# Kernel optimization log

Measured on AMD Instinct MI355X. Metric: run time of the kernel, lower is better.

## Reference

```python
import jax, jax.numpy as jnp
import numpy as np

B, S, H = 2, 2048, 4096
NQ, NKV, D = 32, 8, 128
EPS = 1e-6
THETA = 1000000.0


def rms_norm(x, w, eps=EPS):
    # normalize over last dim (per-head RMSNorm on head_dim)
    var = jnp.mean(jnp.square(x), axis=-1, keepdims=True)
    return x * jax.lax.rsqrt(var + eps) * w


def rope(x, positions, theta=THETA):
    # x: [B, S, N, D]; rotate-half convention (Qwen/Llama style)
    d = x.shape[-1]
    inv_freq = 1.0 / (theta ** (jnp.arange(0, d, 2, dtype=jnp.float32) / d))  # [D/2]
    ang = positions[:, None].astype(jnp.float32) * inv_freq[None, :]          # [S, D/2]
    cos = jnp.cos(ang)[None, :, None, :]
    sin = jnp.sin(ang)[None, :, None, :]
    x1, x2 = x[..., : d // 2], x[..., d // 2 :]
    return jnp.concatenate([x1 * cos - x2 * sin, x2 * cos + x1 * sin], axis=-1)


def setup_inputs() -> dict:
    key = jax.random.key(0)
    ks = jax.random.split(key, 7)
    sc_in = 1.0 / np.sqrt(H)
    sc_out = 1.0 / np.sqrt(NQ * D)
    return {
        "x": jax.random.normal(ks[0], (B, S, H), jnp.float32),
        "wq": jax.random.normal(ks[1], (H, NQ * D), jnp.float32) * sc_in,
        "wk": jax.random.normal(ks[2], (H, NKV * D), jnp.float32) * sc_in,
        "wv": jax.random.normal(ks[3], (H, NKV * D), jnp.float32) * sc_in,
        "wo": jax.random.normal(ks[4], (NQ * D, H), jnp.float32) * sc_out,
        "q_norm_w": jnp.ones((D,), jnp.float32),
        "k_norm_w": jnp.ones((D,), jnp.float32),
    }


def reference(x, wq, wk, wv, wo, q_norm_w, k_norm_w):
    b, s, _ = x.shape
    positions = jnp.arange(s)

    q = (x @ wq).reshape(b, s, NQ, D)   # [B,S,NQ,D]
    k = (x @ wk).reshape(b, s, NKV, D)  # [B,S,NKV,D]
    v = (x @ wv).reshape(b, s, NKV, D)

    # per-head QK RMSNorm, then RoPE
    q = rope(rms_norm(q, q_norm_w), positions)
    k = rope(rms_norm(k, k_norm_w), positions)

    # GQA: expand kv heads to query heads (group = NQ // NKV)
    g = NQ // NKV
    k = jnp.repeat(k, g, axis=2)  # [B,S,NQ,D]
    v = jnp.repeat(v, g, axis=2)

    scale = D ** -0.5
    scores = jnp.einsum("bqhd,bkhd->bhqk", q, k) * scale  # [B,NQ,S,S]
    causal = jnp.tril(jnp.ones((s, s), bool))
    scores = jnp.where(causal[None, None], scores, jnp.finfo(scores.dtype).min)
    attn = jax.nn.softmax(scores, axis=-1)

    out = jnp.einsum("bhqk,bkhd->bqhd", attn, v).reshape(b, s, NQ * D)
    return out @ wo
```

## Files before the change

### kernel.cpp

```cpp
#include <hip/hip_runtime.h>
#include <hip/hip_bf16.h>

#define DEV __device__ __forceinline__

typedef unsigned short u16;
typedef unsigned int u32;
typedef __attribute__((ext_vector_type(8))) short short8;
typedef __attribute__((ext_vector_type(4))) float f32x4;
typedef __attribute__((ext_vector_type(16))) float f32x16;

static constexpr int Bb = 2, Ss = 2048, Hh = 4096, NQ = 32, NKV = 8, Dd = 128;
static constexpr int Mm = Bb * Ss;

DEV u16 f2bf(float f) {
    u32 u = __float_as_uint(f);
    u32 r = (u + 0x7fffu + ((u >> 16) & 1u)) >> 16;
    return (u16)r;
}
DEV float bf2f(u16 b) { return __uint_as_float((u32)b << 16); }
DEV u32 cvtpk(float lo, float hi) {
    u32 r;
    asm("v_cvt_pk_bf16_f32 %0, %1, %2" : "=v"(r) : "v"(lo), "v"(hi));
    return r;
}

__global__ void k_cast(const float4* __restrict__ in, ushort4* __restrict__ out, int n4) {
    int i = blockIdx.x * 256 + threadIdx.x;
    if (i < n4) {
        float4 v = in[i];
        ushort4 o;
        o.x = f2bf(v.x); o.y = f2bf(v.y); o.z = f2bf(v.z); o.w = f2bf(v.w);
        out[i] = o;
    }
}

__global__ void k_transpose(const float* __restrict__ in, u16* __restrict__ out, int R, int C) {
    __shared__ float t[32][33];
    int lx = threadIdx.x & 31, ly = threadIdx.x >> 5;
    long tc = (long)blockIdx.x * 32, tr = (long)blockIdx.y * 32;
    #pragma unroll
    for (int i = 0; i < 32; i += 8) t[ly + i][lx] = in[(tr + ly + i) * C + tc + lx];
    __syncthreads();
    #pragma unroll
    for (int i = 0; i < 32; i += 8) out[(tc + ly + i) * R + tr + lx] = f2bf(t[lx][ly + i]);
}

DEV void gld16(const void* g, void* l) {
    __builtin_amdgcn_global_load_lds((const __attribute__((address_space(1))) void*)g,
                                     (__attribute__((address_space(3))) void*)l, 16, 0, 0);
}

#define FENCE asm volatile("" ::: "memory")

template <int MODE>
__global__ __launch_bounds__(512) void k_gemm256(const u16* __restrict__ A, const u16* __restrict__ BT,
                                                 void* __restrict__ Cp, int M, int N, int K) {
    __shared__ u16 S[2][32768];
    const int tid = threadIdx.x, lane = tid & 63, wid = tid >> 6;
    const int wr = wid >> 2, wc = wid & 3;
    const long m0 = (long)blockIdx.y * 256, n0 = (long)blockIdx.x * 256;
    const int r15 = lane & 15;
    const int cch0 = 8 * ((lane >> 4) ^ (r15 & 7));

    const u16 *pA[4], *pB[4];
    {
        int srow = wid * 8 + (lane >> 3);
        int scol = 8 * ((lane & 7) ^ (lane >> 3));
        #pragma unroll
        for (int j = 0; j < 4; j++) {
            pA[j] = A + (m0 + j * 64 + srow) * (long)K + scol;
            pB[j] = BT + (n0 + j * 64 + srow) * (long)K + scol;
        }
    }

    f32x4 acc[8][4];
    #pragma unroll
    for (int i = 0; i < 8; i++)
        #pragma unroll
        for (int j = 0; j < 4; j++) acc[i][j] = f32x4{0.f, 0.f, 0.f, 0.f};

    const int NT = K / 64;
    auto STAGE_A = [&](int t) {
        int tb = t & 1; long ko = (long)t * 64;
        #pragma unroll
        for (int j = 0; j < 4; j++) gld16(pA[j] + ko, (void*)&S[tb][j * 4096 + wid * 512]);
    };
    auto STAGE_B = [&](int t) {
        int tb = t & 1; long ko = (long)t * 64;
        #pragma unroll
        for (int j = 0; j < 4; j++) gld16(pB[j] + ko, (void*)&S[tb][16384 + j * 4096 + wid * 512]);
    };

    const int aro = wr * 8192 + r15 * 64 + cch0;
    const int bro = 16384 + (wc >> 1) * 8192 + (wc & 1) * 4096 + r15 * 64 + cch0;

    STAGE_B(0); STAGE_A(0); STAGE_B(1); STAGE_A(1);
    asm volatile("s_waitcnt vmcnt(8)" ::: "memory");
    FENCE; __builtin_amdgcn_s_barrier(); FENCE;

    short8 af[4][2], b01[2][2], b23[2][2];
    for (int kt = 0; kt < NT; ++kt) {
        const u16* Sb = S[kt & 1];
        #pragma unroll
        for (int m = 0; m < 4; m++) {
            af[m][0] = *(const short8*)&Sb[aro + m * 1024];
            af[m][1] = *(const short8*)&Sb[(aro + m * 1024) ^ 32];
        }
        #pragma unroll
        for (int n = 0; n < 2; n++) {
            b01[n][0] = *(const short8*)&Sb[bro + n * 1024];
            b01[n][1] = *(const short8*)&Sb[(bro + n * 1024) ^ 32];
        }
        FENCE; __builtin_amdgcn_s_barrier(); FENCE;
        __builtin_amdgcn_s_setprio(1);
        #pragma unroll
        for (int m = 0; m < 4; m++)
            #pragma unroll
            for (int n = 0; n < 2; n++) {
                acc[m][n] = __builtin_amdgcn_mfma_f32_16x16x32_bf16(af[m][0], b01[n][0], acc[m][n], 0, 0, 0);
                acc[m][n] = __builtin_amdgcn_mfma_f32_16x16x32_bf16(af[m][1], b01[n][1], acc[m][n], 0, 0, 0);
            }
        __builtin_amdgcn_s_setprio(0);
        FENCE; __builtin_amdgcn_s_barrier(); FENCE;
        #pragma unroll
        for (int n = 0; n < 2; n++) {
            b23[n][0] = *(const short8*)&Sb[bro + (n + 2) * 1024];
            b23[n][1] = *(const short8*)&Sb[(bro + (n + 2) * 1024) ^ 32];
        }
        FENCE; __builtin_amdgcn_s_barrier(); FENCE;
        __builtin_amdgcn_s_setprio(1);
        #pragma unroll
        for (int m = 0; m < 4; m++)
            #pragma unroll
            for (int n = 0; n < 2; n++) {
                acc[m][n + 2] = __builtin_amdgcn_mfma_f32_16x16x32_bf16(af[m][0], b23[n][0], acc[m][n + 2], 0, 0, 0);
                acc[m][n + 2] = __builtin_amdgcn_mfma_f32_16x16x32_bf16(af[m][1], b23[n][1], acc[m][n + 2], 0, 0, 0);
            }
        __builtin_amdgcn_s_setprio(0);
        FENCE; __builtin_amdgcn_s_barrier(); FENCE;
        if (kt + 2 < NT) STAGE_B(kt + 2);
        #pragma unroll
        for (int m = 0; m < 4; m++) {
            af[m][0] = *(const short8*)&Sb[aro + (m + 4) * 1024];
            af[m][1] = *(const short8*)&Sb[(aro + (m + 4) * 1024) ^ 32];
        }
        FENCE; __builtin_amdgcn_s_barrier(); FENCE;
        __builtin_amdgcn_s_setprio(1);
        #pragma unroll
        for (int m = 0; m < 4; m++)
            #pragma unroll
            for (int n = 0; n < 2; n++) {
                acc[m + 4][n] = __builtin_amdgcn_mfma_f32_16x16x32_bf16(af[m][0], b01[n][0], acc[m + 4][n], 0, 0, 0);
                acc[m + 4][n] = __builtin_amdgcn_mfma_f32_16x16x32_bf16(af[m][1], b01[n][1], acc[m + 4][n], 0, 0, 0);
            }
        __builtin_amdgcn_s_setprio(0);
        FENCE; __builtin_amdgcn_s_barrier(); FENCE;
        if (kt + 2 < NT) {
            STAGE_A(kt + 2);
            asm volatile("s_waitcnt vmcnt(8)" ::: "memory");
        } else {
            asm volatile("s_waitcnt vmcnt(0)" ::: "memory");
        }
        FENCE; __builtin_amdgcn_s_barrier(); FENCE;
        __builtin_amdgcn_s_setprio(1);
        #pragma unroll
        for (int m = 0; m < 4; m++)
            #pragma unroll
            for (int n = 0; n < 2; n++) {
                acc[m + 4][n + 2] = __builtin_amdgcn_mfma_f32_16x16x32_bf16(af[m][0], b23[n][0], acc[m + 4][n + 2], 0, 0, 0);
                acc[m + 4][n + 2] = __builtin_amdgcn_mfma_f32_16x16x32_bf16(af[m][1], b23[n][1], acc[m + 4][n + 2], 0, 0, 0);
            }
        __builtin_amdgcn_s_setprio(0);
        FENCE; __builtin_amdgcn_s_barrier(); FENCE;
    }

    const int rq = (lane >> 4) * 4;
    #pragma unroll
    for (int m = 0; m < 8; m++) {
        #pragma unroll
        for (int n = 0; n < 4; n++) {
            long row0 = m0 + wr * 128 + m * 16 + rq;
            long col = n0 + wc * 64 + n * 16 + r15;
            if (MODE == 0) {
                float* Cf = (float*)Cp;
                #pragma unroll
                for (int i = 0; i < 4; i++) Cf[(row0 + i) * N + col] = acc[m][n][i];
            } else {
                u16* Cb = (u16*)Cp;
                #pragma unroll
                for (int i = 0; i < 4; i++) Cb[(row0 + i) * N + col] = f2bf(acc[m][n][i]);
            }
        }
    }
}

template <int MODE>
__global__ __launch_bounds__(256) void k_gemm_bt(const u16* __restrict__ A, const u16* __restrict__ BT,
                                                 void* __restrict__ Cp, int M, int N, int K) {
    __shared__ u16 As[4096];
    __shared__ u16 Bs[4096];
    int tid = threadIdx.x, lane = tid & 63, wid = tid >> 6;
    int wr = wid >> 1, wc = wid & 1;
    long m0 = (long)blockIdx.y * 128, n0 = (long)blockIdx.x * 128;
    const f32x4 fz = {0.f, 0.f, 0.f, 0.f};
    f32x4 acc[4][4];
    #pragma unroll
    for (int i = 0; i < 4; i++)
        #pragma unroll
        for (int j = 0; j < 4; j++) acc[i][j] = fz;

    const u16* gA = A + (m0 + (tid >> 2)) * K + (tid & 3) * 8;
    const u16* gB = BT + (n0 + (tid >> 2)) * K + (tid & 3) * 8;
    u16* lA0 = As + wid * 512;
    u16* lA1 = As + 2048 + wid * 512;
    u16* lB0 = Bs + wid * 512;
    u16* lB1 = Bs + 2048 + wid * 512;
    int r15 = lane & 15, khalf = (lane >> 4) * 8;
    long rowoff = (long)64 * K;

    for (int kt = 0; kt < K; kt += 32) {
        gld16(gA + kt, lA0);
        gld16(gA + kt + rowoff, lA1);
        gld16(gB + kt, lB0);
        gld16(gB + kt + rowoff, lB1);
        __syncthreads();
        short8 av[4], bv[4];
        #pragma unroll
        for (int f = 0; f < 4; f++) {
            av[f] = *(const short8*)&As[(wr * 64 + f * 16 + r15) * 32 + khalf];
            bv[f] = *(const short8*)&Bs[(wc * 64 + f * 16 + r15) * 32 + khalf];
        }
        #pragma unroll
        for (int i = 0; i < 4; i++)
            #pragma unroll
            for (int j = 0; j < 4; j++)
                acc[i][j] = __builtin_amdgcn_mfma_f32_16x16x32_bf16(av[i], bv[j], acc[i][j], 0, 0, 0);
        __syncthreads();
    }

    int rq = (lane >> 4) * 4;
    #pragma unroll
    for (int mf = 0; mf < 4; mf++) {
        #pragma unroll
        for (int nf = 0; nf < 4; nf++) {
            long row0 = m0 + wr * 64 + mf * 16 + rq;
            long col = n0 + wc * 64 + nf * 16 + r15;
            if (MODE == 1) {
                u16* Cb = (u16*)Cp;
                ushort4 pk;
                pk.x = f2bf(acc[mf][nf][0]);
                pk.y = f2bf(acc[mf][nf][1]);
                pk.z = f2bf(acc[mf][nf][2]);
                pk.w = f2bf(acc[mf][nf][3]);
                *(ushort4*)&Cb[col * M + row0] = pk;
            } else {
                u16* Cb = (u16*)Cp;
                #pragma unroll
                for (int i = 0; i < 4; i++) Cb[(row0 + i) * N + col] = f2bf(acc[mf][nf][i]);
            }
        }
    }
}

__global__ __launch_bounds__(256) void k_normrope(u16* __restrict__ buf,
                                                  const float* __restrict__ w, int NH, float oscale) {
    int row = blockIdx.x * 4 + (threadIdx.x >> 6);
    int lane = threadIdx.x & 63;
    long base = (long)row * 128;
    float x1 = bf2f(buf[base + lane]), x2 = bf2f(buf[base + lane + 64]);
    float ss = x1 * x1 + x2 * x2;
    #pragma unroll
    for (int m = 1; m < 64; m <<= 1) ss += __shfl_xor(ss, m);
    float r = rsqrtf(ss * (1.f / 128.f) + 1e-6f);
    float n1 = x1 * r * w[lane], n2 = x2 * r * w[lane + 64];
    int pos = (row / NH) % Ss;
    float invf = exp2f((float)lane * (-19.931568569324174f / 64.f));
    float ang = (float)pos * invf;
    float c = cosf(ang), sn = sinf(ang);
    buf[base + lane] = f2bf((n1 * c - n2 * sn) * oscale);
    buf[base + lane + 64] = f2bf((n2 * c + n1 * sn) * oscale);
}

__global__ __launch_bounds__(256, 2) void k_attn(const u16* __restrict__ Q, const u16* __restrict__ Kb,
                                                 const u16* __restrict__ Vg, u16* __restrict__ O) {
    __shared__ u16 KT[2][64 * 128];
    __shared__ u16 VT[2][128 * 64];
    int tid = threadIdx.x, lane = tid & 63, wid = tid >> 6;
    int b = blockIdx.z;
    int hk = blockIdx.y;
    int h = hk * 4 + wid;
    int pr = blockIdx.x;
    int q0a = pr * 32;
    int q0b = (63 - pr) * 32;
    int c31 = lane & 31, hi5 = lane >> 5;
    int kx16 = (c31 & 15) << 3;
    int kx8 = (c31 & 7) << 3;

    short8 qfa[8], qfb[8];
    {
        const u16* qra = Q + ((long)(b * Ss + q0a + c31) * NQ + h) * Dd + hi5 * 8;
        const u16* qrb = Q + ((long)(b * Ss + q0b + c31) * NQ + h) * Dd + hi5 * 8;
        #pragma unroll
        for (int c = 0; c < 8; c++) {
            qfa[c] = *(const short8*)(qra + c * 16);
            qfb[c] = *(const short8*)(qrb + c * 16);
        }
    }

    const u16* kg[4];
    const u16* vg[4];
    int i0 = wid * 4;
    #pragma unroll
    for (int ii = 0; ii < 4; ii++) {
        int i = i0 + ii;
        int r = i * 4 + (lane >> 4);
        kg[ii] = Kb + ((long)(b * Ss + r) * NKV + hk) * Dd + 8 * ((lane & 15) ^ (r & 15));
        int d = i * 8 + (lane >> 3);
        vg[ii] = Vg + (long)(hk * Dd + d) * Mm + (long)b * Ss + 8 * ((lane & 7) ^ (d & 7));
    }

    f32x16 oaa[4], oab[4];
    #pragma unroll
    for (int f = 0; f < 4; f++)
        #pragma unroll
        for (int r = 0; r < 16; r++) { oaa[f][r] = 0.f; oab[f][r] = 0.f; }
    float mra = -INFINITY, lra = 0.f, mrb = -INFINITY, lrb = 0.f;

    const long kadv = (long)64 * NKV * Dd;
    int nt = q0b / 64 + 1;
    int cur = 0;

    auto STEP = [&](int k0, int q0, const short8 (&qf)[8], f32x16 (&oa)[4],
                    float& mrun, float& lrun) {
        int ql = q0 + c31;
        int krow = k0 & 32;
        f32x16 st;
        #pragma unroll
        for (int r = 0; r < 16; r++) st[r] = 0.f;
        __builtin_amdgcn_s_setprio(1);
        #pragma unroll
        for (int c = 0; c < 8; c++) {
            short8 kf = *(const short8*)&KT[cur][(krow + c31) * 128 + ((c * 16 + hi5 * 8) ^ kx16)];
            st = __builtin_amdgcn_mfma_f32_32x32x16_bf16(kf, qf[c], st, 0, 0, 0);
        }
        __builtin_amdgcn_s_setprio(0);
        float p[16];
        if (k0 + 31 > q0) {
            #pragma unroll
            for (int r = 0; r < 16; r++) {
                int kidx = k0 + (r & 3) + 8 * (r >> 2) + 4 * hi5;
                p[r] = (kidx > ql) ? -INFINITY : st[r];
            }
        } else {
            #pragma unroll
            for (int r = 0; r < 16; r++) p[r] = st[r];
        }
        float pmax = p[0];
        #pragma unroll
        for (int r = 1; r < 16; r++) pmax = fmaxf(pmax, p[r]);
        pmax = fmaxf(pmax, __shfl_xor(pmax, 32));
        if (!__all(pmax - mrun <= 8.f)) {
            float mnew = fmaxf(mrun, pmax);
            float sc = __builtin_amdgcn_exp2f(mrun - mnew);
            lrun *= sc;
            #pragma unroll
            for (int f = 0; f < 4; f++)
                #pragma unroll
                for (int r = 0; r < 16; r++) oa[f][r] *= sc;
            mrun = mnew;
        }
        float ls = 0.f;
        #pragma unroll
        for (int r = 0; r < 16; r++) {
            float e = __builtin_amdgcn_exp2f(p[r] - mrun);
            p[r] = e;
            ls += e;
        }
        ls += __shfl_xor(ls, 32);
        lrun += ls;

        u32 w0 = cvtpk(p[0], p[1]), w1 = cvtpk(p[2], p[3]);
        u32 w2 = cvtpk(p[4], p[5]), w3 = cvtpk(p[6], p[7]);
        u32 w4 = cvtpk(p[8], p[9]), w5 = cvtpk(p[10], p[11]);
        u32 w6 = cvtpk(p[12], p[13]), w7 = cvtpk(p[14], p[15]);
        u32 x0 = (u32)__shfl_xor((int)w0, 32), x1 = (u32)__shfl_xor((int)w1, 32);
        u32 x2 = (u32)__shfl_xor((int)w2, 32), x3 = (u32)__shfl_xor((int)w3, 32);
        u32 x4 = (u32)__shfl_xor((int)w4, 32), x5 = (u32)__shfl_xor((int)w5, 32);
        u32 x6 = (u32)__shfl_xor((int)w6, 32), x7 = (u32)__shfl_xor((int)w7, 32);
        union { u32 u[4]; short8 s; } pb0, pb1;
        if (hi5) {
            pb0.u[0] = x2; pb0.u[1] = x3; pb0.u[2] = w2; pb0.u[3] = w3;
            pb1.u[0] = x6; pb1.u[1] = x7; pb1.u[2] = w6; pb1.u[3] = w7;
        } else {
            pb0.u[0] = w0; pb0.u[1] = w1; pb0.u[2] = x0; pb0.u[3] = x1;
            pb1.u[0] = w4; pb1.u[1] = w5; pb1.u[2] = x4; pb1.u[3] = x5;
        }
        __builtin_amdgcn_s_setprio(1);
        #pragma unroll
        for (int f = 0; f < 4; f++) {
            int d = 32 * f + c31;
            const u16* vrow = &VT[cur][d * 64];
            short8 v0 = *(const short8*)&vrow[(krow + hi5 * 8) ^ kx8];
            short8 v1 = *(const short8*)&vrow[(krow + 16 + hi5 * 8) ^ kx8];
            oa[f] = __builtin_amdgcn_mfma_f32_32x32x16_bf16(v0, pb0.s, oa[f], 0, 0, 0);
            oa[f] = __builtin_amdgcn_mfma_f32_32x32x16_bf16(v1, pb1.s, oa[f], 0, 0, 0);
        }
        __builtin_amdgcn_s_setprio(0);
    };

    #pragma unroll
    for (int ii = 0; ii < 4; ii++) {
        gld16(kg[ii], &KT[0][(i0 + ii) * 512]);
        gld16(vg[ii], &VT[0][(i0 + ii) * 512]);
    }
    __syncthreads();

    for (int t = 0; t < nt; ++t) {
        if (t + 1 < nt) {
            long ko = (long)(t + 1) * kadv;
            int vo = (t + 1) * 64;
            #pragma unroll
            for (int ii = 0; ii < 4; ii++) {
                gld16(kg[ii] + ko, &KT[cur ^ 1][(i0 + ii) * 512]);
                gld16(vg[ii] + vo, &VT[cur ^ 1][(i0 + ii) * 512]);
            }
        }
        #pragma unroll
        for (int ks = 0; ks < 2; ++ks) {
            int k0 = t * 64 + ks * 32;
            if (k0 <= q0a + 31) STEP(k0, q0a, qfa, oaa, mra, lra);
            if (k0 <= q0b + 31) STEP(k0, q0b, qfb, oab, mrb, lrb);
        }
        __syncthreads();
        cur ^= 1;
    }

    #pragma unroll
    for (int x = 0; x < 2; x++) {
        int q0 = x ? q0b : q0a;
        f32x16* oa = x ? oab : oaa;
        float linv = 1.f / (x ? lrb : lra);
        u16* orow = O + ((long)(b * Ss + q0 + c31) * NQ + h) * Dd;
        #pragma unroll
        for (int f = 0; f < 4; f++) {
            #pragma unroll
            for (int rq = 0; rq < 4; rq++) {
                int dbase = 32 * f + 8 * rq + 4 * hi5;
                union { u32 u[2]; ushort4 v; } pk;
                pk.u[0] = cvtpk(oa[f][4 * rq + 0] * linv, oa[f][4 * rq + 1] * linv);
                pk.u[1] = cvtpk(oa[f][4 * rq + 2] * linv, oa[f][4 * rq + 3] * linv);
                *(ushort4*)(orow + dbase) = pk.v;
            }
        }
    }
}

extern "C" void kernel_launch(void* const* d_in, const int* in_sizes, int n_in,
                              void* d_out, int out_size, void* d_ws, size_t ws_size,
                              hipStream_t stream) {
    (void)in_sizes; (void)n_in; (void)out_size; (void)ws_size;
    const float* x = (const float*)d_in[0];
    const float* wq = (const float*)d_in[1];
    const float* wk = (const float*)d_in[2];
    const float* wv = (const float*)d_in[3];
    const float* wo = (const float*)d_in[4];
    const float* qnw = (const float*)d_in[5];
    const float* knw = (const float*)d_in[6];

    char* ws = (char*)d_ws;
    const size_t MB = 1024 * 1024;
    u16* xb = (u16*)(ws);
    u16* W  = (u16*)(ws + 32 * MB);
    u16* qb = (u16*)(ws + 64 * MB);
    u16* kb = (u16*)(ws + 96 * MB);
    u16* vt = (u16*)(ws + 104 * MB);
    u16* ao = xb;

    int n4 = Mm * Hh / 4;
    k_cast<<<n4 / 256, 256, 0, stream>>>((const float4*)x, (ushort4*)xb, n4);

    k_transpose<<<dim3(Hh / 32, Hh / 32), 256, 0, stream>>>(wq, W, Hh, Hh);
    k_gemm256<2><<<dim3(Hh / 256, Mm / 256), 512, 0, stream>>>(xb, W, qb, Mm, Hh, Hh);
    k_normrope<<<(Mm * NQ) / 4, 256, 0, stream>>>(qb, qnw, NQ,
        (float)(0.08838834764831845 * 1.4426950408889634));

    k_transpose<<<dim3((NKV * Dd) / 32, Hh / 32), 256, 0, stream>>>(wk, W, Hh, NKV * Dd);
    k_gemm_bt<2><<<dim3((NKV * Dd) / 128, Mm / 128), 256, 0, stream>>>(xb, W, kb, Mm, NKV * Dd, Hh);
    k_normrope<<<(Mm * NKV) / 4, 256, 0, stream>>>(kb, knw, NKV, 1.0f);

    k_transpose<<<dim3((NKV * Dd) / 32, Hh / 32), 256, 0, stream>>>(wv, W, Hh, NKV * Dd);
    k_gemm_bt<1><<<dim3((NKV * Dd) / 128, Mm / 128), 256, 0, stream>>>(xb, W, vt, Mm, NKV * Dd, Hh);

    k_attn<<<dim3(32, NKV, Bb), 256, 0, stream>>>(qb, kb, vt, ao);

    k_transpose<<<dim3(Hh / 32, Hh / 32), 256, 0, stream>>>(wo, W, Hh, Hh);
    k_gemm256<0><<<dim3(Hh / 256, Mm / 256), 512, 0, stream>>>(ao, W, d_out, Mm, Hh, NQ * Dd);
}
```

Measured before the change: 646.1 us.

## Fuse Q, K, V projections into a single 256-tile GEMM launch

New measurement: 568.3 us. 12.0% less time.

```diff
diff --git a/kernel.cpp b/kernel.cpp
--- a/kernel.cpp
+++ b/kernel.cpp
@@ -53,8 +53,10 @@
 #define FENCE asm volatile("" ::: "memory")
 
 template <int MODE>
-__global__ __launch_bounds__(512) void k_gemm256(const u16* __restrict__ A, const u16* __restrict__ BT,
-                                                 void* __restrict__ Cp, int M, int N, int K) {
+__global__ __launch_bounds__(512) void k_gemm256(const u16* __restrict__ A, const u16* __restrict__ B0,
+                                                 const u16* __restrict__ B1, void* __restrict__ C0,
+                                                 void* __restrict__ C1, void* __restrict__ C2,
+                                                 int M, int N, int K) {
     __shared__ u16 S[2][32768];
     const int tid = threadIdx.x, lane = tid & 63, wid = tid >> 6;
     const int wr = wid >> 2, wc = wid & 3;
@@ -62,6 +64,10 @@
     const int r15 = lane & 15;
     const int cch0 = 8 * ((lane >> 4) ^ (r15 & 7));
 
+    const u16* Bbase = B0;
+    long nb0 = n0;
+    if (MODE == 3 && blockIdx.x >= 16) { Bbase = B1; nb0 = n0 - 4096; }
+
     const u16 *pA[4], *pB[4];
     {
         int srow = wid * 8 + (lane >> 3);
@@ -69,7 +75,7 @@
         #pragma unroll
         for (int j = 0; j < 4; j++) {
             pA[j] = A + (m0 + j * 64 + srow) * (long)K + scol;
-            pB[j] = BT + (n0 + j * 64 + srow) * (long)K + scol;
+            pB[j] = Bbase + (nb0 + j * 64 + srow) * (long)K + scol;
         }
     }
 
@@ -182,13 +188,33 @@
             long row0 = m0 + wr * 128 + m * 16 + rq;
             long col = n0 + wc * 64 + n * 16 + r15;
             if (MODE == 0) {
-                float* Cf = (float*)Cp;
+                float* Cf = (float*)C0;
                 #pragma unroll
                 for (int i = 0; i < 4; i++) Cf[(row0 + i) * N + col] = acc[m][n][i];
-            } else {
-                u16* Cb = (u16*)Cp;
+            } else if (MODE == 2) {
+                u16* Cb = (u16*)C0;
                 #pragma unroll
                 for (int i = 0; i < 4; i++) Cb[(row0 + i) * N + col] = f2bf(acc[m][n][i]);
+            } else {
+                if (blockIdx.x < 16) {
+                    u16* Cb = (u16*)C0;
+                    #pragma unroll
+                    for (int i = 0; i < 4; i++) Cb[(row0 + i) * 4096 + col] = f2bf(acc[m][n][i]);
+                } else if (blockIdx.x < 20) {
+                    u16* Cb = (u16*)C1;
+                    long cl = col - 4096;
+                    #pragma unroll
+                    for (int i = 0; i < 4; i++) Cb[(row0 + i) * 1024 + cl] = f2bf(acc[m][n][i]);
+                } else {
+                    u16* Cb = (u16*)C2;
+                    long cl = col - 5120;
+                    ushort4 pk;
+                    pk.x = f2bf(acc[m][n][0]);
+                    pk.y = f2bf(acc[m][n][1]);
+                    pk.z = f2bf(acc[m][n][2]);
+                    pk.w = f2bf(acc[m][n][3]);
+                    *(ushort4*)&Cb[cl * Mm + row0] = pk;
+                }
             }
         }
     }
@@ -458,7 +484,7 @@
 extern "C" void kernel_launch(void* const* d_in, const int* in_sizes, int n_in,
                               void* d_out, int out_size, void* d_ws, size_t ws_size,
                               hipStream_t stream) {
-    (void)in_sizes; (void)n_in; (void)out_size; (void)ws_size;
+    (void)in_sizes; (void)n_in; (void)out_size;
     const float* x = (const float*)d_in[0];
     const float* wq = (const float*)d_in[1];
     const float* wk = (const float*)d_in[2];
@@ -469,8 +495,10 @@
 
     char* ws = (char*)d_ws;
     const size_t MB = 1024 * 1024;
+    const float qscale = (float)(0.08838834764831845 * 1.4426950408889634);
+
     u16* xb = (u16*)(ws);
-    u16* W  = (u16*)(ws + 32 * MB);
+    u16* Wq = (u16*)(ws + 32 * MB);
     u16* qb = (u16*)(ws + 64 * MB);
     u16* kb = (u16*)(ws + 96 * MB);
     u16* vt = (u16*)(ws + 104 * MB);
@@ -479,20 +507,33 @@
     int n4 = Mm * Hh / 4;
     k_cast<<<n4 / 256, 256, 0, stream>>>((const float4*)x, (ushort4*)xb, n4);
 
-    k_transpose<<<dim3(Hh / 32, Hh / 32), 256, 0, stream>>>(wq, W, Hh, Hh);
-    k_gemm256<2><<<dim3(Hh / 256, Mm / 256), 512, 0, stream>>>(xb, W, qb, Mm, Hh, Hh);
-    k_normrope<<<(Mm * NQ) / 4, 256, 0, stream>>>(qb, qnw, NQ,
-        (float)(0.08838834764831845 * 1.4426950408889634));
-
-    k_transpose<<<dim3((NKV * Dd) / 32, Hh / 32), 256, 0, stream>>>(wk, W, Hh, NKV * Dd);
-    k_gemm_bt<2><<<dim3((NKV * Dd) / 128, Mm / 128), 256, 0, stream>>>(xb, W, kb, Mm, NKV * Dd, Hh);
-    k_normrope<<<(Mm * NKV) / 4, 256, 0, stream>>>(kb, knw, NKV, 1.0f);
-
-    k_transpose<<<dim3((NKV * Dd) / 32, Hh / 32), 256, 0, stream>>>(wv, W, Hh, NKV * Dd);
-    k_gemm_bt<1><<<dim3((NKV * Dd) / 128, Mm / 128), 256, 0, stream>>>(xb, W, vt, Mm, NKV * Dd, Hh);
+    if (ws_size >= 128 * MB) {
+        u16* Wkv = (u16*)(ws + 112 * MB);
+        u16* WkT = Wkv;
+        u16* WvT = Wkv + (size_t)1024 * 4096;
+        k_transpose<<<dim3(Hh / 32, Hh / 32), 256, 0, stream>>>(wq, Wq, Hh, Hh);
+        k_transpose<<<dim3((NKV * Dd) / 32, Hh / 32), 256, 0, stream>>>(wk, WkT, Hh, NKV * Dd);
+        k_transpose<<<dim3((NKV * Dd) / 32, Hh / 32), 256, 0, stream>>>(wv, WvT, Hh, NKV * Dd);
+
+        k_gemm256<3><<<dim3(24, Mm / 256), 512, 0, stream>>>(xb, Wq, Wkv, qb, kb, vt, Mm, 6144, Hh);
+
+        k_normrope<<<(Mm * NQ) / 4, 256, 0, stream>>>(qb, qnw, NQ, qscale);
+        k_normrope<<<(Mm * NKV) / 4, 256, 0, stream>>>(kb, knw, NKV, 1.0f);
+    } else {
+        k_transpose<<<dim3(Hh / 32, Hh / 32), 256, 0, stream>>>(wq, Wq, Hh, Hh);
+        k_gemm256<2><<<dim3(Hh / 256, Mm / 256), 512, 0, stream>>>(xb, Wq, nullptr, qb, nullptr, nullptr, Mm, Hh, Hh);
+        k_normrope<<<(Mm * NQ) / 4, 256, 0, stream>>>(qb, qnw, NQ, qscale);
+
+        k_transpose<<<dim3((NKV * Dd) / 32, Hh / 32), 256, 0, stream>>>(wk, Wq, Hh, NKV * Dd);
+        k_gemm_bt<2><<<dim3((NKV * Dd) / 128, Mm / 128), 256, 0, stream>>>(xb, Wq, kb, Mm, NKV * Dd, Hh);
+        k_normrope<<<(Mm * NKV) / 4, 256, 0, stream>>>(kb, knw, NKV, 1.0f);
+
+        k_transpose<<<dim3((NKV * Dd) / 32, Hh / 32), 256, 0, stream>>>(wv, Wq, Hh, NKV * Dd);
+        k_gemm_bt<1><<<dim3((NKV * Dd) / 128, Mm / 128), 256, 0, stream>>>(xb, Wq, vt, Mm, NKV * Dd, Hh);
+    }
 
     k_attn<<<dim3(32, NKV, Bb), 256, 0, stream>>>(qb, kb, vt, ao);
 
-    k_transpose<<<dim3(Hh / 32, Hh / 32), 256, 0, stream>>>(wo, W, Hh, Hh);
-    k_gemm256<0><<<dim3(Hh / 256, Mm / 256), 512, 0, stream>>>(ao, W, d_out, Mm, Hh, NQ * Dd);
-}
+    k_transpose<<<dim3(Hh / 32, Hh / 32), 256, 0, stream>>>(wo, Wq, Hh, Hh);
+    k_gemm256<0><<<dim3(Hh / 256, Mm / 256), 512, 0, stream>>>(ao, Wq, nullptr, d_out, nullptr, nullptr, Mm, Hh, NQ * Dd);
+}
```
